# Kernel tuning notes

Measured on AMD Instinct MI355X. Metric: run time of the kernel, lower is better.

The kernel has to match this reference:

```python
import jax, jax.numpy as jnp
import numpy as np

B_, L_, DM, DI, DS, DTR, DC = 1, 2048, 2048, 4096, 16, 128, 4


def setup_inputs() -> dict:
    key = jax.random.key(0)
    ks = jax.random.split(key, 8)
    s = lambda k, shape, scale: jax.random.normal(k, shape, jnp.float32) * scale
    inp = {
        "hidden_states": s(ks[0], (B_, L_, DM), 1.0),
        "in_proj_weight": s(ks[1], (2 * DI, DM), DM ** -0.5),
        "conv1d_weight": s(ks[2], (DI, 1, DC), DC ** -0.5),
        "x_proj_weight": s(ks[3], (DTR + 2 * DS, DI), DI ** -0.5),
        "dt_proj_weight": s(ks[4], (DI, DTR), DTR ** -0.5),
        "out_proj_weight": s(ks[5], (DM, DI), DI ** -0.5),
    }
    # dt_proj_bias = inverse-softplus of dt ~ LogUniform[1e-3, 0.1] (as in init_dtprojbias)
    dt = jnp.exp(jax.random.uniform(ks[6], (DI,), jnp.float32) * (np.log(0.1) - np.log(0.001)) + np.log(0.001))
    dt = jnp.clip(dt, 1e-4, None)
    inp["dt_proj_bias"] = dt + jnp.log(-jnp.expm1(-dt))
    # A_log init: log of repeat(arange(1, d_state+1)) per d_inner row
    inp["A_log"] = jnp.log(jnp.tile(jnp.arange(1, DS + 1, dtype=jnp.float32), (DI, 1)))
    inp["D"] = jnp.ones((DI,), jnp.float32)
    return inp


def reference(hidden_states, in_proj_weight, conv1d_weight, x_proj_weight,
              dt_proj_weight, dt_proj_bias, A_log, D, out_proj_weight):
    b, l, dm = hidden_states.shape
    di, ds = A_log.shape
    # in_proj: [b,l,dm] -> xz [b, 2*di, l]
    xz = jnp.einsum('ed,bld->bel', in_proj_weight, hidden_states)
    x, z = xz[:, :di], xz[:, di:]
    # depthwise causal conv1d (pad left d_conv-1, no bias) + SiLU
    x = jax.lax.conv_general_dilated(
        x, conv1d_weight, window_strides=(1,), padding=[(DC - 1, 0)],
        dimension_numbers=('NCH', 'OIH', 'NCH'), feature_group_count=di)
    x = jax.nn.silu(x)  # [b, di, l]
    # x_proj -> dt, B, C
    x_dbl = jnp.einsum('pd,bdl->blp', x_proj_weight, x)  # [b,l,dtr+2*ds]
    dt, Bc, Cc = jnp.split(x_dbl, [DTR, DTR + ds], axis=-1)
    delta = jnp.einsum('dr,blr->bld', dt_proj_weight, dt) + dt_proj_bias
    delta = jax.nn.softplus(delta)  # delta_softplus=True, delta_bias applied
    A = -jnp.exp(A_log)  # [di, ds]
    u = jnp.transpose(x, (0, 2, 1))  # [b,l,di]

    def step(h, inputs):
        d_t, B_t, C_t, u_t = inputs  # [b,di],[b,ds],[b,ds],[b,di]
        dA = jnp.exp(d_t[..., None] * A)                      # [b,di,ds]
        h = h * dA + (d_t * u_t)[..., None] * B_t[:, None, :]  # [b,di,ds]
        y = jnp.einsum('bdn,bn->bd', h, C_t)
        return h, y

    h0 = jnp.zeros((b, di, ds), hidden_states.dtype)
    xs = (jnp.swapaxes(delta, 0, 1), jnp.swapaxes(Bc, 0, 1),
          jnp.swapaxes(Cc, 0, 1), jnp.swapaxes(u, 0, 1))
    _, ys = jax.lax.scan(step, h0, xs)          # [l,b,di]
    y = jnp.swapaxes(ys, 0, 1) + u * D          # skip term u*D
    y = y * jax.nn.silu(jnp.transpose(z, (0, 2, 1)))  # gate
    return jnp.einsum('md,bld->blm', out_proj_weight, y)
```

## Files before the change

### kernel.cpp

```cpp
#include <hip/hip_runtime.h>
#include <hip/hip_bf16.h>

#define LSEQ 2048
#define DMODEL 2048
#define DINNER 4096
#define DSTATE 16
#define DTRANK 128
#define DCONV 4
#define DXP (DTRANK + 2*DSTATE)
#define NCHUNK 64
#define LCHUNK (LSEQ / NCHUNK)
#define KSPLIT 16
#define OKS 4

using bf16 = __hip_bfloat16;
typedef __attribute__((ext_vector_type(8))) short short8;
typedef __attribute__((ext_vector_type(4))) float float4v;

__device__ __forceinline__ float b2f(bf16 v) { return __bfloat162float(v); }
__device__ __forceinline__ bf16 f2b(float v) { return __float2bfloat16(v); }
__device__ __forceinline__ float bl16(unsigned u) { return __uint_as_float(u << 16); }
__device__ __forceinline__ float bh16(unsigned u) { return __uint_as_float(u & 0xffff0000u); }

__device__ __forceinline__ short f2bs(float v) {
    bf16 b = __float2bfloat16(v);
    union { bf16 b; short s; } u; u.b = b; return u.s;
}

__device__ __forceinline__ float fsilu(float x) {
    return x * __builtin_amdgcn_rcpf(1.0f + __expf(-x));
}

__device__ __forceinline__ short8 ld8(const float* p) {
    float4v f0 = *(const float4v*)p;
    float4v f1 = *(const float4v*)(p + 4);
    short8 r;
    r[0] = f2bs(f0[0]); r[1] = f2bs(f0[1]); r[2] = f2bs(f0[2]); r[3] = f2bs(f0[3]);
    r[4] = f2bs(f1[0]); r[5] = f2bs(f1[1]); r[6] = f2bs(f1[2]); r[7] = f2bs(f1[3]);
    return r;
}
__device__ __forceinline__ short8 ld8(const bf16* p) { return *(const short8*)p; }

template<typename CT> __device__ __forceinline__ CT cvtC(float v);
template<> __device__ __forceinline__ bf16  cvtC<bf16>(float v)  { return f2b(v); }
template<> __device__ __forceinline__ float cvtC<float>(float v) { return v; }

template<typename T> __device__ __forceinline__ float cvtL(T v);
template<> __device__ __forceinline__ float cvtL<bf16>(bf16 v)   { return b2f(v); }
template<> __device__ __forceinline__ float cvtL<float>(float v) { return v; }

__device__ __forceinline__ void glds16(const bf16* g, void* lds_base) {
    __builtin_amdgcn_global_load_lds(
        (const __attribute__((address_space(1))) void*)g,
        (__attribute__((address_space(3))) void*)lds_base, 16, 0, 0);
}

__global__ __launch_bounds__(256) void cvt3(
    const float* __restrict__ s0, bf16* __restrict__ d0, int n0,
    const float* __restrict__ s1, bf16* __restrict__ d1, int n1,
    const float* __restrict__ s2, bf16* __restrict__ d2, int n2)
{
    const int b = blockIdx.x;
    const int nb0 = n0 >> 11, nb1 = n1 >> 11;
    const float* s; bf16* d; int i;
    if (b < nb0)            { s = s0; d = d0; i = b * 2048; }
    else if (b < nb0 + nb1) { s = s1; d = d1; i = (b - nb0) * 2048; }
    else                    { s = s2; d = d2; i = (b - nb0 - nb1) * 2048; }
    i += threadIdx.x * 8;
    *(short8*)(d + i) = ld8(s + i);
}

__global__ __launch_bounds__(256) void cvt1(
    const float* __restrict__ src, bf16* __restrict__ dst, int n)
{
    int i = (blockIdx.x * 256 + threadIdx.x) * 8;
    if (i >= n) return;
    *(short8*)(dst + i) = ld8(src + i);
}

#define GBAR  __builtin_amdgcn_s_barrier()
#define VMW4  asm volatile("s_waitcnt vmcnt(4)" ::: "memory")
#define VMW0  asm volatile("s_waitcnt vmcnt(0)" ::: "memory")

#define LDA8(BASE, RB, AF) do {                                                \
  _Pragma("unroll") for (int mi_ = 0; mi_ < 4; ++mi_)                          \
  _Pragma("unroll") for (int kk_ = 0; kk_ < 2; ++kk_)                          \
    AF[mi_][kk_] = *(const short8*)((BASE) + (((RB) + mi_*16 + t16) << 6)      \
                                    + ((((kk_*4) + quad) ^ sw7) << 3));        \
} while (0)

#define LDB4(BASE, RB, BF) do {                                                \
  _Pragma("unroll") for (int nj_ = 0; nj_ < 2; ++nj_)                          \
  _Pragma("unroll") for (int kk_ = 0; kk_ < 2; ++kk_)                          \
    BF[nj_][kk_] = *(const short8*)((BASE) + (((RB) + nj_*16 + t16) << 6)      \
                                    + ((((kk_*4) + quad) ^ sw7) << 3));        \
} while (0)

#define MM16(AF, BF, MO, NO) do {                                              \
  _Pragma("unroll") for (int kk_ = 0; kk_ < 2; ++kk_)                          \
  _Pragma("unroll") for (int mi_ = 0; mi_ < 4; ++mi_)                          \
  _Pragma("unroll") for (int nj_ = 0; nj_ < 2; ++nj_)                          \
    acc[(MO)+mi_][(NO)+nj_] = __builtin_amdgcn_mfma_f32_16x16x32_bf16(         \
        AF[mi_][kk_], BF[nj_][kk_], acc[(MO)+mi_][(NO)+nj_], 0, 0, 0);         \
} while (0)

#define ST_ALO(tau) do { size_t ko_ = (size_t)(tau) << 6; int bo_ = ((tau)&1) << 15; \
  glds16(sA +       ko_, dA0 + bo_);                                           \
  glds16(sA + oA1 + ko_, dA1 + bo_); } while (0)
#define ST_AHI(tau) do { size_t ko_ = (size_t)(tau) << 6; int bo_ = ((tau)&1) << 15; \
  glds16(sA + oA2 + ko_, dA2 + bo_);                                           \
  glds16(sA + oA3 + ko_, dA3 + bo_); } while (0)
#define ST_BLO(tau) do { size_t ko_ = (size_t)(tau) << 6; int bo_ = ((tau)&1) << 15; \
  glds16(sB +       ko_, dB0 + bo_);                                           \
  glds16(sB + oB1 + ko_, dB1 + bo_); } while (0)
#define ST_BHI(tau) do { size_t ko_ = (size_t)(tau) << 6; int bo_ = ((tau)&1) << 15; \
  glds16(sB + oB2 + ko_, dB2 + bo_);                                           \
  glds16(sB + oB3 + ko_, dB3 + bo_); } while (0)

#define KSTEP(T, BI) do {                                                      \
    const bf16* Ab = As[BI];                                                   \
    const bf16* Bb = Bs[BI];                                                   \
    short8 af[4][2], b0[2][2], b1[2][2];                                       \
                                       \
    LDA8(Ab, wm, af);                                                          \
    LDB4(Bb, wn, b0);                                                          \
    if ((T) + 1 < NT) { ST_AHI((T) + 1); ST_BLO((T) + 1); }                    \
    __builtin_amdgcn_s_setprio(1); MM16(af, b0, 0, 0);                         \
    __builtin_amdgcn_s_setprio(0); GBAR;                                       \
                    \
    LDB4(Bb, wn + 32, b1);                                                     \
    if ((T) + 2 < NT) ST_ALO((T) + 2);                                         \
    __builtin_amdgcn_s_setprio(1); MM16(af, b1, 0, 2);                         \
    __builtin_amdgcn_s_setprio(0); GBAR;                                       \
                           \
    LDA8(Ab, wm + 64, af);                                                     \
    if ((T) + 2 < NT) ST_BHI((T) + 2);                                         \
    __builtin_amdgcn_s_setprio(1); MM16(af, b1, 4, 2);                         \
    __builtin_amdgcn_s_setprio(0); GBAR;                                       \
                                   \
    __builtin_amdgcn_s_setprio(1); MM16(af, b0, 4, 0);                         \
    __builtin_amdgcn_s_setprio(0);                                             \
    if ((T) + 2 < NT) { VMW4; } else { VMW0; }                                 \
    GBAR;                                                                      \
} while (0)

#define GEMM_PRO_COMMON                                                        \
    const int t    = threadIdx.x;                                              \
    const int wave = t >> 6;                                                   \
    const int lane = t & 63;                                                   \
    const int t16  = lane & 15;                                                \
    const int quad = lane >> 4;                                                \
    const int sw7  = t16 & 7;                                                  \
    const int wm   = (wave >> 2) * 128;                                        \
    const int wn   = (wave & 3) * 64;                                          \
    const int lrow  = lane >> 3;                                               \
    const int lseg  = lane & 7;                                                \
    const int segx  = (lseg ^ lrow) * 8;                                       \
    const int bwoff = (wave & 3) * 8 + (wave >> 2) * 64;

#define GEMM_LDS_DSTS                                                          \
    char* dA0 = (char*)&As[0][(  0 + wave * 8) * 64];                          \
    char* dA1 = (char*)&As[0][(128 + wave * 8) * 64];                          \
    char* dA2 = (char*)&As[0][( 64 + wave * 8) * 64];                          \
    char* dA3 = (char*)&As[0][(192 + wave * 8) * 64];                          \
    char* dB0 = (char*)&Bs[0][(  0 + bwoff) * 64];                             \
    char* dB1 = (char*)&Bs[0][(128 + bwoff) * 64];                             \
    char* dB2 = (char*)&Bs[0][( 32 + bwoff) * 64];                             \
    char* dB3 = (char*)&Bs[0][(160 + bwoff) * 64];

__global__ __launch_bounds__(512, 2) void gemm_inproj(
    const bf16* __restrict__ A, int lda,
    const bf16* __restrict__ B, int ldb,
    bf16* __restrict__ C, int ldc, int K)
{
    __shared__ __align__(16) bf16 As[2][256 * 64];
    __shared__ __align__(16) bf16 Bs[2][256 * 64];
    GEMM_PRO_COMMON
    const int bid = blockIdx.x;
    const int s   = (bid & 7) * (gridDim.x >> 3) + (bid >> 3);
    const int bm0 = (s & 7) << 8;
    const int bn0 = (s >> 3) << 8;

    const bf16* sA = A + (size_t)(bm0 + wave * 8 + lrow) * lda + segx;
    const bf16* sB = B + (size_t)(bn0 + bwoff + lrow) * ldb + segx;
    const size_t oA1 = (size_t)128 * lda, oA2 = (size_t)64 * lda, oA3 = (size_t)192 * lda;
    const size_t oB1 = (size_t)128 * ldb, oB2 = (size_t)32 * ldb, oB3 = (size_t)160 * ldb;
    GEMM_LDS_DSTS

    const int NT = K >> 6;

    float4v acc[8][4];
#pragma unroll
    for (int i = 0; i < 8; ++i)
#pragma unroll
        for (int j = 0; j < 4; ++j) acc[i][j] = (float4v)(0.0f);

    ST_ALO(0); ST_AHI(0); ST_BLO(0); ST_BHI(0);
    if (NT > 1) { ST_ALO(1); ST_BHI(1); VMW4; } else { VMW0; }
    GBAR;

    for (int T = 0; T < NT; T += 2) {
        KSTEP(T, 0);
        KSTEP(T + 1, 1);
    }

#pragma unroll
    for (int mi = 0; mi < 8; ++mi) {
#pragma unroll
        for (int nj = 0; nj < 4; ++nj) {
            const int m_base = bm0 + wm + (mi >> 2) * 64 + (mi & 3) * 16 + quad * 4;
            const int n_g    = bn0 + wn + (nj >> 1) * 32 + (nj & 1) * 16 + t16;
#pragma unroll
            for (int r = 0; r < 4; ++r)
                C[(size_t)(m_base + r) * ldc + n_g] = f2b(acc[mi][nj][r]);
        }
    }
}

__global__ __launch_bounds__(512, 2) void gemm_outproj(
    const bf16* __restrict__ A, int lda,
    const bf16* __restrict__ B, int ldb,
    float* __restrict__ P, int ldc, int Kc)
{
    __shared__ __align__(16) bf16 As[2][256 * 64];
    __shared__ __align__(16) bf16 Bs[2][256 * 64];
    GEMM_PRO_COMMON
    const int bid = blockIdx.x;
    const int s   = (bid & 7) * (gridDim.x >> 3) + (bid >> 3);
    const int bm0 = (s & 7) << 8;
    const int t2  = s >> 3;
    const int bn0 = (t2 & 7) << 8;
    const int ks  = t2 >> 3;

    const bf16* sA = A + (size_t)(bm0 + wave * 8 + lrow) * lda + segx + (size_t)ks * Kc;
    const bf16* sB = B + (size_t)(bn0 + bwoff + lrow) * ldb + segx + (size_t)ks * Kc;
    const size_t oA1 = (size_t)128 * lda, oA2 = (size_t)64 * lda, oA3 = (size_t)192 * lda;
    const size_t oB1 = (size_t)128 * ldb, oB2 = (size_t)32 * ldb, oB3 = (size_t)160 * ldb;
    GEMM_LDS_DSTS

    const int NT = Kc >> 6;

    float4v acc[8][4];
#pragma unroll
    for (int i = 0; i < 8; ++i)
#pragma unroll
        for (int j = 0; j < 4; ++j) acc[i][j] = (float4v)(0.0f);

    ST_ALO(0); ST_AHI(0); ST_BLO(0); ST_BHI(0);
    if (NT > 1) { ST_ALO(1); ST_BHI(1); VMW4; } else { VMW0; }
    GBAR;

    for (int T = 0; T < NT; T += 2) {
        KSTEP(T, 0);
        KSTEP(T + 1, 1);
    }

    float* Pk = P + (size_t)ks * 2048 * (size_t)ldc;
#pragma unroll
    for (int mi = 0; mi < 8; ++mi) {
#pragma unroll
        for (int nj = 0; nj < 4; ++nj) {
            const int m_base = bm0 + wm + (mi >> 2) * 64 + (mi & 3) * 16 + quad * 4;
            const int n_g    = bn0 + wn + (nj >> 1) * 32 + (nj & 1) * 16 + t16;
#pragma unroll
            for (int r = 0; r < 4; ++r)
                Pk[(size_t)(m_base + r) * ldc + n_g] = acc[mi][nj][r];
        }
    }
}

__global__ __launch_bounds__(256) void reduce4f(
    const float* __restrict__ P, float* __restrict__ out, int MN)
{
    int i = (blockIdx.x * 256 + threadIdx.x) * 4;
    if (i >= MN) return;
    float4v s = *(const float4v*)(P + i);
#pragma unroll
    for (int ks = 1; ks < OKS; ++ks) {
        float4v v = *(const float4v*)(P + (size_t)ks * MN + i);
#pragma unroll
        for (int j = 0; j < 4; ++j) s[j] += v[j];
    }
    *(float4v*)(out + i) = s;
}

template<int BN, typename CT, bool SP>
__global__ __launch_bounds__(256) void gemm_glds64(
    const bf16* __restrict__ A, int lda,
    const bf16* __restrict__ B, int ldb,
    CT* __restrict__ C, int ldc,
    int K, const float* __restrict__ bias)
{
    constexpr int NJ  = BN / 32;
    constexpr int BGL = BN / 32;
    __shared__ bf16 As[128][64];
    __shared__ bf16 Bs[BN][64];

    const int t    = threadIdx.x;
    const int wave = t >> 6;
    const int lane = t & 63;
    const int t16  = lane & 15;
    const int quad = lane >> 4;
    const int wm   = (wave >> 1) * 64;
    const int wn   = (wave & 1) * (BN / 2);
    const int bm0  = blockIdx.x * 128;
    const int bn0  = blockIdx.y * BN;

    const int lrow = lane >> 3;
    const int gseg = (((lane & 7) ^ lrow) * 8);

    const bf16* Ag[4]; char* Ad[4];
#pragma unroll
    for (int g = 0; g < 4; g++) {
        Ag[g] = A + (size_t)(bm0 + wave * 32 + g * 8 + lrow) * lda + gseg;
        Ad[g] = (char*)As + (wave * 32 + g * 8) * 128;
    }
    const bf16* Bg[BGL]; char* Bd[BGL];
#pragma unroll
    for (int g = 0; g < BGL; g++) {
        int r = (BN == 128) ? (wave * 32 + g * 8) : (wave * 16 + g * 8);
        Bg[g] = B + (size_t)(bn0 + r + lrow) * ldb + gseg;
        Bd[g] = (char*)Bs + r * 128;
    }

    float4v acc[4][NJ];
#pragma unroll
    for (int i = 0; i < 4; i++)
#pragma unroll
        for (int j = 0; j < NJ; j++) acc[i][j] = (float4v)(0.0f);

    const int sw = t16 & 7;

    for (int k0 = 0; k0 < K; k0 += 64) {
        __syncthreads();
#pragma unroll
        for (int g = 0; g < 4; g++)   glds16(Ag[g] + k0, Ad[g]);
#pragma unroll
        for (int g = 0; g < BGL; g++) glds16(Bg[g] + k0, Bd[g]);
        __syncthreads();

#pragma unroll
        for (int kk = 0; kk < 2; kk++) {
            const int kso = ((kk * 4 + quad) ^ sw) * 8;
            short8 a[4], b[NJ];
#pragma unroll
            for (int mi = 0; mi < 4; mi++)
                a[mi] = *(const short8*)(&As[wm + mi * 16 + t16][kso]);
#pragma unroll
            for (int nj = 0; nj < NJ; nj++)
                b[nj] = *(const short8*)(&Bs[wn + nj * 16 + t16][kso]);
#pragma unroll
            for (int mi = 0; mi < 4; mi++)
#pragma unroll
                for (int nj = 0; nj < NJ; nj++)
                    acc[mi][nj] = __builtin_amdgcn_mfma_f32_16x16x32_bf16(
                        a[mi], b[nj], acc[mi][nj], 0, 0, 0);
        }
    }

#pragma unroll
    for (int mi = 0; mi < 4; mi++) {
#pragma unroll
        for (int nj = 0; nj < NJ; nj++) {
            int n_g = bn0 + wn + nj * 16 + t16;
            float bia = SP ? bias[n_g] : 0.0f;
#pragma unroll
            for (int r = 0; r < 4; r++) {
                int m_g = bm0 + wm + mi * 16 + quad * 4 + r;
                float v = acc[mi][nj][r];
                if (SP) {
                    float x = v + bia;
                    v = (x > 20.0f) ? x : __logf(1.0f + __expf(x));
                }
                C[(size_t)m_g * ldc + n_g] = cvtC<CT>(v);
            }
        }
    }
}

template<typename AT, typename CT, bool SP>
__global__ __launch_bounds__(256) void gemm_bt(
    const AT* __restrict__ A, int lda,
    const float* __restrict__ B, int ldb,
    CT* __restrict__ C, int ldc,
    int M, int N, int K,
    const float* __restrict__ bias)
{
    __shared__ bf16 As[64][40];
    __shared__ bf16 Bs[64][40];

    const int t    = threadIdx.x;
    const int bm0  = blockIdx.x * 64;
    const int bn0  = blockIdx.y * 64;
    const int row  = t >> 2;
    const int seg  = (t & 3) * 8;
    const int wave = t >> 6;
    const int lane = t & 63;
    const int wm   = (wave >> 1) * 32;
    const int wn   = (wave & 1) * 32;
    const int t16  = lane & 15;
    const int quad = lane >> 4;

    float4v acc[2][2];
#pragma unroll
    for (int i = 0; i < 2; i++)
#pragma unroll
        for (int j = 0; j < 2; j++) acc[i][j] = (float4v)(0.0f);

    const AT*    Aptr = A + (size_t)(bm0 + row) * lda + seg;
    const float* Bptr = B + (size_t)(bn0 + row) * ldb + seg;
    const bool a_ok = (bm0 + row) < M;
    const bool b_ok = (bn0 + row) < N;
    const short8 zero8 = (short8)(0);

    for (int k0 = 0; k0 < K; k0 += 32) {
        short8 av = a_ok ? ld8(Aptr + k0) : zero8;
        short8 bv = b_ok ? ld8(Bptr + k0) : zero8;
        __syncthreads();
        *(short8*)(&As[row][seg]) = av;
        *(short8*)(&Bs[row][seg]) = bv;
        __syncthreads();

        short8 a0 = *(const short8*)(&As[wm + t16][quad * 8]);
        short8 a1 = *(const short8*)(&As[wm + 16 + t16][quad * 8]);
        short8 b0 = *(const short8*)(&Bs[wn + t16][quad * 8]);
        short8 b1 = *(const short8*)(&Bs[wn + 16 + t16][quad * 8]);
        acc[0][0] = __builtin_amdgcn_mfma_f32_16x16x32_bf16(a0, b0, acc[0][0], 0, 0, 0);
        acc[0][1] = __builtin_amdgcn_mfma_f32_16x16x32_bf16(a0, b1, acc[0][1], 0, 0, 0);
        acc[1][0] = __builtin_amdgcn_mfma_f32_16x16x32_bf16(a1, b0, acc[1][0], 0, 0, 0);
        acc[1][1] = __builtin_amdgcn_mfma_f32_16x16x32_bf16(a1, b1, acc[1][1], 0, 0, 0);
    }

#pragma unroll
    for (int i = 0; i < 2; i++) {
#pragma unroll
        for (int j = 0; j < 2; j++) {
            int n_g = bn0 + wn + j * 16 + t16;
            if (n_g >= N) continue;
            float bia = SP ? bias[n_g] : 0.0f;
#pragma unroll
            for (int r = 0; r < 4; r++) {
                int m_g = bm0 + wm + i * 16 + quad * 4 + r;
                if (m_g >= M) continue;
                float v = acc[i][j][r];
                if (SP) {
                    float x = v + bia;
                    v = (x > 20.0f) ? x : log1pf(__expf(x));
                }
                C[(size_t)m_g * ldc + n_g] = cvtC<CT>(v);
            }
        }
    }
}

__global__ __launch_bounds__(256) void gemm_bt_splitk(
    const bf16* __restrict__ A, int lda,
    const float* __restrict__ B, int ldb,
    float* __restrict__ P,
    int M, int N, int K)
{
    __shared__ bf16 As[64][40];
    __shared__ bf16 Bs[64][40];

    const int t    = threadIdx.x;
    const int bm0  = blockIdx.x * 64;
    const int bn0  = blockIdx.y * 64;
    const int ks   = blockIdx.z;
    const int KS   = gridDim.z;
    const int kbeg = ks * (K / KS);
    const int kend = kbeg + (K / KS);
    const int row  = t >> 2;
    const int seg  = (t & 3) * 8;
    const int wave = t >> 6;
    const int lane = t & 63;
    const int wm   = (wave >> 1) * 32;
    const int wn   = (wave & 1) * 32;
    const int t16  = lane & 15;
    const int quad = lane >> 4;

    float4v acc[2][2];
#pragma unroll
    for (int i = 0; i < 2; i++)
#pragma unroll
        for (int j = 0; j < 2; j++) acc[i][j] = (float4v)(0.0f);

    const bf16*  Aptr = A + (size_t)(bm0 + row) * lda + seg;
    const float* Bptr = B + (size_t)(bn0 + row) * ldb + seg;
    const bool a_ok = (bm0 + row) < M;
    const bool b_ok = (bn0 + row) < N;
    const short8 zero8 = (short8)(0);

    for (int k0 = kbeg; k0 < kend; k0 += 32) {
        short8 av = a_ok ? ld8(Aptr + k0) : zero8;
        short8 bv = b_ok ? ld8(Bptr + k0) : zero8;
        __syncthreads();
        *(short8*)(&As[row][seg]) = av;
        *(short8*)(&Bs[row][seg]) = bv;
        __syncthreads();

        short8 a0 = *(const short8*)(&As[wm + t16][quad * 8]);
        short8 a1 = *(const short8*)(&As[wm + 16 + t16][quad * 8]);
        short8 b0 = *(const short8*)(&Bs[wn + t16][quad * 8]);
        short8 b1 = *(const short8*)(&Bs[wn + 16 + t16][quad * 8]);
        acc[0][0] = __builtin_amdgcn_mfma_f32_16x16x32_bf16(a0, b0, acc[0][0], 0, 0, 0);
        acc[0][1] = __builtin_amdgcn_mfma_f32_16x16x32_bf16(a0, b1, acc[0][1], 0, 0, 0);
        acc[1][0] = __builtin_amdgcn_mfma_f32_16x16x32_bf16(a1, b0, acc[1][0], 0, 0, 0);
        acc[1][1] = __builtin_amdgcn_mfma_f32_16x16x32_bf16(a1, b1, acc[1][1], 0, 0, 0);
    }

    float* Pk = P + (size_t)ks * M * N;
#pragma unroll
    for (int i = 0; i < 2; i++) {
#pragma unroll
        for (int j = 0; j < 2; j++) {
            int n_g = bn0 + wn + j * 16 + t16;
            if (n_g >= N) continue;
#pragma unroll
            for (int r = 0; r < 4; r++) {
                int m_g = bm0 + wm + i * 16 + quad * 4 + r;
                if (m_g >= M) continue;
                Pk[(size_t)m_g * N + n_g] = acc[i][j][r];
            }
        }
    }
}

__global__ __launch_bounds__(256) void reduce_splitk(
    const float* __restrict__ P, bf16* __restrict__ C, float* __restrict__ bc, int MN)
{
    int i = blockIdx.x * 256 + threadIdx.x;
    if (i >= MN) return;
    float s = 0.f;
#pragma unroll
    for (int ks = 0; ks < KSPLIT; ks++) s += P[(size_t)ks * MN + i];
    C[i] = f2b(s);
    int l = i / DXP;
    int p = i - l * DXP;
    if (p >= DTRANK) bc[l * 32 + (p - DTRANK)] = s;
}

__global__ __launch_bounds__(256) void conv_silu_par(
    const bf16* __restrict__ xz, const float* __restrict__ w, bf16* __restrict__ xc)
{
    const int d  = blockIdx.x * 256 + threadIdx.x;
    const int lc = blockIdx.y * 256;
    const float w0 = w[d * 4 + 0];
    const float w1 = w[d * 4 + 1];
    const float w2 = w[d * 4 + 2];
    const float w3 = w[d * 4 + 3];
    const size_t S = 2 * DINNER;
    const bf16* p = xz + d;
    float xm3 = 0.f, xm2 = 0.f, xm1 = 0.f;
    if (lc >= 3) {
        xm3 = b2f(p[(size_t)(lc - 3) * S]);
        xm2 = b2f(p[(size_t)(lc - 2) * S]);
        xm1 = b2f(p[(size_t)(lc - 1) * S]);
    }
    for (int l = lc; l < lc + 256; ++l) {
        float x0 = b2f(p[(size_t)l * S]);
        float a = w0 * xm3 + w1 * xm2 + w2 * xm1 + w3 * x0;
        xc[(size_t)l * DINNER + d] = f2b(fsilu(a));
        xm3 = xm2; xm2 = xm1; xm1 = x0;
    }
}

__global__ __launch_bounds__(256) void conv_silu_inplace(
    bf16* __restrict__ xz, const float* __restrict__ w)
{
    const int d = blockIdx.x * 256 + threadIdx.x;
    const float w0 = w[d * 4 + 0];
    const float w1 = w[d * 4 + 1];
    const float w2 = w[d * 4 + 2];
    const float w3 = w[d * 4 + 3];
    bf16* p = xz + d;
    const size_t S = 2 * DINNER;
    float xm3 = 0.f, xm2 = 0.f, xm1 = 0.f;
    for (int l = 0; l < LSEQ; l += 4) {
        float x0 = b2f(p[(size_t)(l + 0) * S]);
        float x1 = b2f(p[(size_t)(l + 1) * S]);
        float x2 = b2f(p[(size_t)(l + 2) * S]);
        float x3 = b2f(p[(size_t)(l + 3) * S]);
        float a0 = w0 * xm3 + w1 * xm2 + w2 * xm1 + w3 * x0;
        float a1 = w0 * xm2 + w1 * xm1 + w2 * x0  + w3 * x1;
        float a2 = w0 * xm1 + w1 * x0  + w2 * x1  + w3 * x2;
        float a3 = w0 * x0  + w1 * x1  + w2 * x2  + w3 * x3;
        p[(size_t)(l + 0) * S] = f2b(a0 / (1.0f + __expf(-a0)));
        p[(size_t)(l + 1) * S] = f2b(a1 / (1.0f + __expf(-a1)));
        p[(size_t)(l + 2) * S] = f2b(a2 / (1.0f + __expf(-a2)));
        p[(size_t)(l + 3) * S] = f2b(a3 / (1.0f + __expf(-a3)));
        xm3 = x1; xm2 = x2; xm1 = x3;
    }
}

__global__ __launch_bounds__(256) void scan_chunk1(
    const float* __restrict__ dlt, const bf16* __restrict__ xc,
    const float* __restrict__ bc, const float* __restrict__ A_log,
    float* __restrict__ hend, float* __restrict__ Pbuf)
{
    const int d = blockIdx.x * 256 + threadIdx.x;
    const int c = blockIdx.y;

    float Ac[16];
    {
        const float* ap = A_log + d * DSTATE;
#pragma unroll
        for (int i = 0; i < 16; i++) Ac[i] = -__expf(ap[i]);
    }

    float h[16];
#pragma unroll
    for (int i = 0; i < 16; i++) h[i] = 0.f;
    float sdelta = 0.f;

    const float* pd = dlt + (size_t)c * LCHUNK * DINNER + d;
    const bf16*  pu = xc  + (size_t)c * LCHUNK * DINNER + d;
    const float* pb = bc  + (size_t)c * LCHUNK * 32;

#pragma unroll 2
    for (int l = 0; l < LCHUNK; ++l) {
        const float delta = *pd;
        const float u     = b2f(*pu);
        const float du    = delta * u;
        sdelta += delta;
        float4v B0 = *(const float4v*)pb;
        float4v B1 = *(const float4v*)(pb + 4);
        float4v B2 = *(const float4v*)(pb + 8);
        float4v B3 = *(const float4v*)(pb + 12);
#pragma unroll
        for (int i = 0; i < 16; i++) {
            float dA = __expf(delta * Ac[i]);
            float Bi = (i < 4) ? B0[i] : (i < 8) ? B1[i - 4] : (i < 12) ? B2[i - 8] : B3[i - 12];
            h[i] = h[i] * dA + du * Bi;
        }
        pd += DINNER; pu += DINNER; pb += 32;
    }

    float* hp = hend + ((size_t)c * DINNER + d) * DSTATE;
    float* pp = Pbuf + ((size_t)c * DINNER + d) * DSTATE;
#pragma unroll
    for (int q = 0; q < 4; q++) {
        float4v hv, pv;
#pragma unroll
        for (int j = 0; j < 4; j++) {
            hv[j] = h[q * 4 + j];
            pv[j] = __expf(sdelta * Ac[q * 4 + j]);
        }
        *(float4v*)(hp + q * 4) = hv;
        *(float4v*)(pp + q * 4) = pv;
    }
}

__global__ __launch_bounds__(256) void scan_combine(
    float* __restrict__ hend, const float* __restrict__ Pbuf)
{
    const int dn = blockIdx.x * 256 + threadIdx.x;
    const size_t STR = (size_t)DINNER * DSTATE;
    float H = 0.f;
    size_t idx = dn;
    for (int c0 = 0; c0 < NCHUNK; c0 += 8) {
        float he[8], pp[8];
#pragma unroll
        for (int j = 0; j < 8; j++) {
            he[j] = hend[idx + (size_t)j * STR];
            pp[j] = Pbuf[idx + (size_t)j * STR];
        }
#pragma unroll
        for (int j = 0; j < 8; j++) {
            hend[idx + (size_t)j * STR] = H;
            H = he[j] + pp[j] * H;
        }
        idx += 8 * STR;
    }
}

__global__ __launch_bounds__(256) void scan_chunk2(
    const float* __restrict__ dlt, const bf16* __restrict__ xc,
    bf16* __restrict__ xz, const float* __restrict__ bc,
    const float* __restrict__ A_log, const float* __restrict__ Dp,
    const float* __restrict__ Hin)
{
    const int d = blockIdx.x * 256 + threadIdx.x;
    const int c = blockIdx.y;

    float Ac[16];
    {
        const float* ap = A_log + d * DSTATE;
#pragma unroll
        for (int i = 0; i < 16; i++) Ac[i] = -__expf(ap[i]);
    }
    const float Dv = Dp[d];

    float h[16];
    {
        const float* hp = Hin + ((size_t)c * DINNER + d) * DSTATE;
#pragma unroll
        for (int q = 0; q < 4; q++) {
            float4v hv = *(const float4v*)(hp + q * 4);
#pragma unroll
            for (int j = 0; j < 4; j++) h[q * 4 + j] = hv[j];
        }
    }

    const float* pd = dlt + (size_t)c * LCHUNK * DINNER + d;
    const bf16*  pu = xc  + (size_t)c * LCHUNK * DINNER + d;
    const float* pb = bc  + (size_t)c * LCHUNK * 32;
    bf16*        pz = xz  + (size_t)c * LCHUNK * (2 * DINNER) + DINNER + d;

#pragma unroll 2
    for (int l = 0; l < LCHUNK; ++l) {
        const float delta = *pd;
        const float u     = b2f(*pu);
        const float du    = delta * u;
        float4v B0 = *(const float4v*)pb;
        float4v B1 = *(const float4v*)(pb + 4);
        float4v B2 = *(const float4v*)(pb + 8);
        float4v B3 = *(const float4v*)(pb + 12);
        float4v C0 = *(const float4v*)(pb + 16);
        float4v C1 = *(const float4v*)(pb + 20);
        float4v C2 = *(const float4v*)(pb + 24);
        float4v C3 = *(const float4v*)(pb + 28);
        float yv = 0.f;
#pragma unroll
        for (int i = 0; i < 16; i++) {
            float dA = __expf(delta * Ac[i]);
            float Bi = (i < 4) ? B0[i] : (i < 8) ? B1[i - 4] : (i < 12) ? B2[i - 8] : B3[i - 12];
            float Ci = (i < 4) ? C0[i] : (i < 8) ? C1[i - 4] : (i < 12) ? C2[i - 8] : C3[i - 12];
            h[i] = h[i] * dA + du * Bi;
            yv += h[i] * Ci;
        }
        yv += u * Dv;
        float z = b2f(*pz);
        yv *= fsilu(z);
        *pz = f2b(yv);
        pd += DINNER; pu += DINNER; pb += 32; pz += 2 * DINNER;
    }
}

template<typename DT>
__global__ __launch_bounds__(256) void scan_serial(
    const DT* __restrict__ dlt, bf16* __restrict__ xz,
    const bf16* __restrict__ xdbl,
    const float* __restrict__ A_log, const float* __restrict__ Dp)
{
    const int nq = threadIdx.x & 3;
    const int d  = blockIdx.x * 64 + (threadIdx.x >> 2);
    float Ac[4];
#pragma unroll
    for (int i = 0; i < 4; i++)
        Ac[i] = -__expf(A_log[d * DSTATE + nq * 4 + i]);
    const float Dv = Dp[d];
    float h[4] = {0.f, 0.f, 0.f, 0.f};
    for (int l = 0; l < LSEQ; ++l) {
        const float delta = cvtL<DT>(dlt[(size_t)l * DINNER + d]);
        const float u     = b2f(xz[(size_t)l * (2 * DINNER) + d]);
        const uint2 qb = *(const uint2*)(xdbl + (size_t)l * DXP + DTRANK + nq * 4);
        const uint2 qc = *(const uint2*)(xdbl + (size_t)l * DXP + DTRANK + DSTATE + nq * 4);
        float Bv[4] = { bl16(qb.x), bh16(qb.x), bl16(qb.y), bh16(qb.y) };
        float Cv[4] = { bl16(qc.x), bh16(qc.x), bl16(qc.y), bh16(qc.y) };
        const float du = delta * u;
        float yv = 0.f;
#pragma unroll
        for (int i = 0; i < 4; i++) {
            float dA = __expf(delta * Ac[i]);
            h[i] = h[i] * dA + du * Bv[i];
            yv += h[i] * Cv[i];
        }
        yv += __shfl_xor(yv, 1);
        yv += __shfl_xor(yv, 2);
        if (nq == 0) {
            yv += u * Dv;
            bf16* zp = xz + (size_t)l * (2 * DINNER) + DINNER + d;
            float z = b2f(*zp);
            yv *= z / (1.0f + __expf(-z));
            *zp = f2b(yv);
        }
    }
}

extern "C" void kernel_launch(void* const* d_in, const int* in_sizes, int n_in,
                              void* d_out, int out_size, void* d_ws, size_t ws_size,
                              hipStream_t stream)
{
    const float* hs      = (const float*)d_in[0];
    const float* w_in    = (const float*)d_in[1];
    const float* w_conv  = (const float*)d_in[2];
    const float* w_xproj = (const float*)d_in[3];
    const float* w_dt    = (const float*)d_in[4];
    const float *w_out, *b_dt, *A_log, *Dp;
    if (in_sizes[5] == DMODEL * DINNER) {
        w_out = (const float*)d_in[5];
        b_dt  = (const float*)d_in[6];
        A_log = (const float*)d_in[7];
        Dp    = (const float*)d_in[8];
    } else {
        b_dt  = (const float*)d_in[5];
        A_log = (const float*)d_in[6];
        Dp    = (const float*)d_in[7];
        w_out = (const float*)d_in[8];
    }
    float* out = (float*)d_out;

    const size_t SZ_XZ   = (size_t)LSEQ * 2 * DINNER * sizeof(bf16);
    const size_t SZ_XC   = (size_t)LSEQ * DINNER * sizeof(bf16);
    const size_t SZ_XDBL = (size_t)LSEQ * DXP * sizeof(bf16);
    const size_t SZ_DLTF = (size_t)LSEQ * DINNER * sizeof(float);
    const size_t SZ_HP   = (size_t)NCHUNK * DINNER * DSTATE * sizeof(float);
    const size_t SZ_BC   = (size_t)LSEQ * 32 * sizeof(float);

    char* p = (char*)d_ws;
    bf16* xz = (bf16*)p; p += SZ_XZ;

    const size_t need_fast = SZ_XZ + SZ_XC + SZ_XDBL + SZ_DLTF + 2 * SZ_HP + SZ_BC;
    const bool fast = ws_size >= need_fast;

    dim3 blk(256);

    if (fast) {
        bf16*  xc   = (bf16*)p;  p += SZ_XC;
        bf16*  xdbl = (bf16*)p;  p += SZ_XDBL;
        char*  hpr  = p;         p += SZ_DLTF;
        char*  dreg = p;
        float* dlt  = (float*)hpr;
        float* hend = (float*)dreg;
        float* Pbuf = (float*)(dreg + SZ_HP);
        float* bcb  = (float*)(dreg + 2 * SZ_HP);

        bf16*  w_in_b  = (bf16*)hpr;
        float* xp_part = (float*)hpr;
        bf16*  hs_b    = (bf16*)dreg;
        bf16*  w_dt_b  = (bf16*)(dreg + (size_t)LSEQ * DMODEL * sizeof(bf16));
        bf16*  w_out_b = (bf16*)xc;
        float* p_out   = (float*)hpr;

        {
            int n0 = 2 * DINNER * DMODEL, n1 = LSEQ * DMODEL, n2 = DINNER * DTRANK;
            cvt3<<<dim3((n0 + n1 + n2) / 2048), blk, 0, stream>>>(
                w_in, w_in_b, n0, hs, hs_b, n1, w_dt, w_dt_b, n2);
        }

        gemm_inproj<<<dim3(256), dim3(512), 0, stream>>>(
            hs_b, DMODEL, w_in_b, DMODEL, xz, 2*DINNER, DMODEL);

        conv_silu_par<<<dim3(DINNER/256, LSEQ/256), blk, 0, stream>>>(xz, w_conv, xc);

        gemm_bt_splitk<<<dim3(LSEQ/64, 3, KSPLIT), blk, 0, stream>>>(
            xc, DINNER, w_xproj, DINNER, xp_part, LSEQ, DXP, DINNER);
        reduce_splitk<<<dim3((LSEQ * DXP + 255) / 256), blk, 0, stream>>>(
            xp_part, xdbl, bcb, LSEQ * DXP);

        gemm_glds64<128, float, true><<<dim3(LSEQ/128, DINNER/128), blk, 0, stream>>>(
            xdbl, DXP, w_dt_b, DTRANK, dlt, DINNER, DTRANK, b_dt);

        scan_chunk1<<<dim3(DINNER/256, NCHUNK), blk, 0, stream>>>(
            dlt, xc, bcb, A_log, hend, Pbuf);
        scan_combine<<<dim3(DINNER*DSTATE/256), blk, 0, stream>>>(hend, Pbuf);
        scan_chunk2<<<dim3(DINNER/256, NCHUNK), blk, 0, stream>>>(
            dlt, xc, xz, bcb, A_log, Dp, hend);

        cvt1<<<dim3((DMODEL*DINNER)/2048), blk, 0, stream>>>(w_out, w_out_b, DMODEL*DINNER);
        gemm_outproj<<<dim3(256), dim3(512), 0, stream>>>(
            xz + DINNER, 2*DINNER, w_out_b, DINNER, p_out, DMODEL, DINNER/OKS);
        reduce4f<<<dim3(LSEQ*DMODEL/1024), blk, 0, stream>>>(
            p_out, out, LSEQ*DMODEL);
    } else {
        bf16* xdbl = (bf16*)p; p += SZ_XDBL;
        size_t used = (size_t)(p - (char*)d_ws);
        bool dlt_f32 = (ws_size - used) >= SZ_DLTF;

        gemm_bt<float, bf16, false><<<dim3(LSEQ/64, (2*DINNER)/64), blk, 0, stream>>>(
            hs, DMODEL, w_in, DMODEL, xz, 2*DINNER, LSEQ, 2*DINNER, DMODEL, nullptr);
        conv_silu_inplace<<<dim3(DINNER/256), blk, 0, stream>>>(xz, w_conv);
        gemm_bt<bf16, bf16, false><<<dim3(LSEQ/64, 3), blk, 0, stream>>>(
            xz, 2*DINNER, w_xproj, DINNER, xdbl, DXP, LSEQ, DXP, DINNER, nullptr);
        if (dlt_f32) {
            float* dlt = (float*)p;
            gemm_bt<bf16, float, true><<<dim3(LSEQ/64, DINNER/64), blk, 0, stream>>>(
                xdbl, DXP, w_dt, DTRANK, dlt, DINNER, LSEQ, DINNER, DTRANK, b_dt);
            scan_serial<float><<<dim3(DINNER/64), blk, 0, stream>>>(dlt, xz, xdbl, A_log, Dp);
        } else {
            bf16* dlt = (bf16*)p;
            gemm_bt<bf16, bf16, true><<<dim3(LSEQ/64, DINNER/64), blk, 0, stream>>>(
                xdbl, DXP, w_dt, DTRANK, dlt, DINNER, LSEQ, DINNER, DTRANK, b_dt);
            scan_serial<bf16><<<dim3(DINNER/64), blk, 0, stream>>>(dlt, xz, xdbl, A_log, Dp);
        }
        gemm_bt<bf16, float, false><<<dim3(LSEQ/64, DMODEL/64), blk, 0, stream>>>(
            xz + DINNER, 2*DINNER, w_out, DINNER, out, DMODEL, LSEQ, DMODEL, DINNER, nullptr);
    }
}
```

Baseline: 425.8 us.

## Replace x_proj split-K GEMM with swizzled 128x160 LDS-direct kernel and bf16 weight

Replaces the small 64x64 split-K x_proj GEMM with a new kernel that tiles 128 rows by the full 160 output columns, loads A and B straight into LDS with global_load_lds and XOR swizzling, and uses a 4x5 MFMA accumulator tile per wave. This removes the wasted padded third N-tile and the per-lane fp32-to-bf16 loads. The x_proj weight is now converted to bf16 once inside the fused conversion kernel, which grows to four sources. The conv+SiLU kernel gets a finer sequence split (64 instead of 256 rows per block) for more parallelism, at the cost of extra halo reads.

```diff
diff --git a/kernel.cpp b/kernel.cpp
--- a/kernel.cpp
+++ b/kernel.cpp
@@ -55,17 +55,19 @@
         (__attribute__((address_space(3))) void*)lds_base, 16, 0, 0);
 }
 
-__global__ __launch_bounds__(256) void cvt3(
+__global__ __launch_bounds__(256) void cvt4(
     const float* __restrict__ s0, bf16* __restrict__ d0, int n0,
     const float* __restrict__ s1, bf16* __restrict__ d1, int n1,
-    const float* __restrict__ s2, bf16* __restrict__ d2, int n2)
+    const float* __restrict__ s2, bf16* __restrict__ d2, int n2,
+    const float* __restrict__ s3, bf16* __restrict__ d3, int n3)
 {
     const int b = blockIdx.x;
-    const int nb0 = n0 >> 11, nb1 = n1 >> 11;
+    const int nb0 = n0 >> 11, nb1 = n1 >> 11, nb2 = n2 >> 11;
     const float* s; bf16* d; int i;
-    if (b < nb0)            { s = s0; d = d0; i = b * 2048; }
-    else if (b < nb0 + nb1) { s = s1; d = d1; i = (b - nb0) * 2048; }
-    else                    { s = s2; d = d2; i = (b - nb0 - nb1) * 2048; }
+    if (b < nb0)                  { s = s0; d = d0; i = b * 2048; }
+    else if (b < nb0 + nb1)       { s = s1; d = d1; i = (b - nb0) * 2048; }
+    else if (b < nb0 + nb1 + nb2) { s = s2; d = d2; i = (b - nb0 - nb1) * 2048; }
+    else                          { s = s3; d = d3; i = (b - nb0 - nb1 - nb2) * 2048; }
     i += threadIdx.x * 8;
     *(short8*)(d + i) = ld8(s + i);
 }
@@ -284,6 +286,92 @@
     *(float4v*)(out + i) = s;
 }
 
+__global__ __launch_bounds__(256) void gemm_xproj(
+    const bf16* __restrict__ A, int lda,
+    const bf16* __restrict__ B, int ldb,
+    float* __restrict__ P)
+{
+    __shared__ bf16 As[128][64];
+    __shared__ bf16 Bs[160][64];
+
+    const int t    = threadIdx.x;
+    const int wave = t >> 6;
+    const int lane = t & 63;
+    const int t16  = lane & 15;
+    const int quad = lane >> 4;
+    const int wm   = (wave >> 1) * 64;
+    const int wn   = (wave & 1) * 80;
+    const int bm0  = blockIdx.x * 128;
+    const int kbeg = blockIdx.y * (DINNER / KSPLIT);
+
+    const int lrow = lane >> 3;
+    const int gseg = ((lane & 7) ^ lrow) * 8;
+
+    const bf16* Ag[4]; char* Ad[4];
+#pragma unroll
+    for (int g = 0; g < 4; g++) {
+        int r = wave * 32 + g * 8;
+        Ag[g] = A + (size_t)(bm0 + r + lrow) * lda + gseg + kbeg;
+        Ad[g] = (char*)As + r * 128;
+    }
+    const bf16* Bg[5]; char* Bd[5];
+#pragma unroll
+    for (int g = 0; g < 5; g++) {
+        int r = wave * 40 + g * 8;
+        Bg[g] = B + (size_t)(r + lrow) * ldb + gseg + kbeg;
+        Bd[g] = (char*)Bs + r * 128;
+    }
+
+    float4v acc[4][5];
+#pragma unroll
+    for (int i = 0; i < 4; i++)
+#pragma unroll
+        for (int j = 0; j < 5; j++) acc[i][j] = (float4v)(0.0f);
+
+    const int sw = t16 & 7;
+
+    for (int k0 = 0; k0 < DINNER / KSPLIT; k0 += 64) {
+        __syncthreads();
+#pragma unroll
+        for (int g = 0; g < 4; g++) glds16(Ag[g] + k0, Ad[g]);
+#pragma unroll
+        for (int g = 0; g < 5; g++) glds16(Bg[g] + k0, Bd[g]);
+        __syncthreads();
+
+#pragma unroll
+        for (int kk = 0; kk < 2; kk++) {
+            const int kso = ((kk * 4 + quad) ^ sw) * 8;
+            short8 a[4], b[5];
+#pragma unroll
+            for (int mi = 0; mi < 4; mi++)
+                a[mi] = *(const short8*)(&As[wm + mi * 16 + t16][kso]);
+#pragma unroll
+            for (int nj = 0; nj < 5; nj++)
+                b[nj] = *(const short8*)(&Bs[wn + nj * 16 + t16][kso]);
+#pragma unroll
+            for (int mi = 0; mi < 4; mi++)
+#pragma unroll
+                for (int nj = 0; nj < 5; nj++)
+                    acc[mi][nj] = __builtin_amdgcn_mfma_f32_16x16x32_bf16(
+                        a[mi], b[nj], acc[mi][nj], 0, 0, 0);
+        }
+    }
+
+    float* Pk = P + (size_t)blockIdx.y * LSEQ * DXP;
+#pragma unroll
+    for (int mi = 0; mi < 4; mi++) {
+#pragma unroll
+        for (int nj = 0; nj < 5; nj++) {
+            int n_g = wn + nj * 16 + t16;
+#pragma unroll
+            for (int r = 0; r < 4; r++) {
+                int m_g = bm0 + wm + mi * 16 + quad * 4 + r;
+                Pk[(size_t)m_g * DXP + n_g] = acc[mi][nj][r];
+            }
+        }
+    }
+}
+
 template<int BN, typename CT, bool SP>
 __global__ __launch_bounds__(256) void gemm_glds64(
     const bf16* __restrict__ A, int lda,
@@ -453,78 +541,6 @@
     }
 }
 
-__global__ __launch_bounds__(256) void gemm_bt_splitk(
-    const bf16* __restrict__ A, int lda,
-    const float* __restrict__ B, int ldb,
-    float* __restrict__ P,
-    int M, int N, int K)
-{
-    __shared__ bf16 As[64][40];
-    __shared__ bf16 Bs[64][40];
-
-    const int t    = threadIdx.x;
-    const int bm0  = blockIdx.x * 64;
-    const int bn0  = blockIdx.y * 64;
-    const int ks   = blockIdx.z;
-    const int KS   = gridDim.z;
-    const int kbeg = ks * (K / KS);
-    const int kend = kbeg + (K / KS);
-    const int row  = t >> 2;
-    const int seg  = (t & 3) * 8;
-    const int wave = t >> 6;
-    const int lane = t & 63;
-    const int wm   = (wave >> 1) * 32;
-    const int wn   = (wave & 1) * 32;
-    const int t16  = lane & 15;
-    const int quad = lane >> 4;
-
-    float4v acc[2][2];
-#pragma unroll
-    for (int i = 0; i < 2; i++)
-#pragma unroll
-        for (int j = 0; j < 2; j++) acc[i][j] = (float4v)(0.0f);
-
-    const bf16*  Aptr = A + (size_t)(bm0 + row) * lda + seg;
-    const float* Bptr = B + (size_t)(bn0 + row) * ldb + seg;
-    const bool a_ok = (bm0 + row) < M;
-    const bool b_ok = (bn0 + row) < N;
-    const short8 zero8 = (short8)(0);
-
-    for (int k0 = kbeg; k0 < kend; k0 += 32) {
-        short8 av = a_ok ? ld8(Aptr + k0) : zero8;
-        short8 bv = b_ok ? ld8(Bptr + k0) : zero8;
-        __syncthreads();
-        *(short8*)(&As[row][seg]) = av;
-        *(short8*)(&Bs[row][seg]) = bv;
-        __syncthreads();
-
-        short8 a0 = *(const short8*)(&As[wm + t16][quad * 8]);
-        short8 a1 = *(const short8*)(&As[wm + 16 + t16][quad * 8]);
-        short8 b0 = *(const short8*)(&Bs[wn + t16][quad * 8]);
-        short8 b1 = *(const short8*)(&Bs[wn + 16 + t16][quad * 8]);
-        acc[0][0] = __builtin_amdgcn_mfma_f32_16x16x32_bf16(a0, b0, acc[0][0], 0, 0, 0);
-        acc[0][1] = __builtin_amdgcn_mfma_f32_16x16x32_bf16(a0, b1, acc[0][1], 0, 0, 0);
-        acc[1][0] = __builtin_amdgcn_mfma_f32_16x16x32_bf16(a1, b0, acc[1][0], 0, 0, 0);
-        acc[1][1] = __builtin_amdgcn_mfma_f32_16x16x32_bf16(a1, b1, acc[1][1], 0, 0, 0);
-    }
-
-    float* Pk = P + (size_t)ks * M * N;
-#pragma unroll
-    for (int i = 0; i < 2; i++) {
-#pragma unroll
-        for (int j = 0; j < 2; j++) {
-            int n_g = bn0 + wn + j * 16 + t16;
-            if (n_g >= N) continue;
-#pragma unroll
-            for (int r = 0; r < 4; r++) {
-                int m_g = bm0 + wm + i * 16 + quad * 4 + r;
-                if (m_g >= M) continue;
-                Pk[(size_t)m_g * N + n_g] = acc[i][j][r];
-            }
-        }
-    }
-}
-
 __global__ __launch_bounds__(256) void reduce_splitk(
     const float* __restrict__ P, bf16* __restrict__ C, float* __restrict__ bc, int MN)
 {
@@ -543,7 +559,7 @@
     const bf16* __restrict__ xz, const float* __restrict__ w, bf16* __restrict__ xc)
 {
     const int d  = blockIdx.x * 256 + threadIdx.x;
-    const int lc = blockIdx.y * 256;
+    const int lc = blockIdx.y * 64;
     const float w0 = w[d * 4 + 0];
     const float w1 = w[d * 4 + 1];
     const float w2 = w[d * 4 + 2];
@@ -556,7 +572,7 @@
         xm2 = b2f(p[(size_t)(lc - 2) * S]);
         xm1 = b2f(p[(size_t)(lc - 1) * S]);
     }
-    for (int l = lc; l < lc + 256; ++l) {
+    for (int l = lc; l < lc + 64; ++l) {
         float x0 = b2f(p[(size_t)l * S]);
         float a = w0 * xm3 + w1 * xm2 + w2 * xm1 + w3 * x0;
         xc[(size_t)l * DINNER + d] = f2b(fsilu(a));
@@ -829,22 +845,25 @@
         float* xp_part = (float*)hpr;
         bf16*  hs_b    = (bf16*)dreg;
         bf16*  w_dt_b  = (bf16*)(dreg + (size_t)LSEQ * DMODEL * sizeof(bf16));
+        bf16*  w_xp_b  = (bf16*)(dreg + (size_t)LSEQ * DMODEL * sizeof(bf16)
+                                      + (size_t)DINNER * DTRANK * sizeof(bf16));
         bf16*  w_out_b = (bf16*)xc;
         float* p_out   = (float*)hpr;
 
         {
-            int n0 = 2 * DINNER * DMODEL, n1 = LSEQ * DMODEL, n2 = DINNER * DTRANK;
-            cvt3<<<dim3((n0 + n1 + n2) / 2048), blk, 0, stream>>>(
-                w_in, w_in_b, n0, hs, hs_b, n1, w_dt, w_dt_b, n2);
+            int n0 = 2 * DINNER * DMODEL, n1 = LSEQ * DMODEL;
+            int n2 = DINNER * DTRANK,     n3 = DXP * DINNER;
+            cvt4<<<dim3((n0 + n1 + n2 + n3) / 2048), blk, 0, stream>>>(
+                w_in, w_in_b, n0, hs, hs_b, n1, w_dt, w_dt_b, n2, w_xproj, w_xp_b, n3);
         }
 
         gemm_inproj<<<dim3(256), dim3(512), 0, stream>>>(
             hs_b, DMODEL, w_in_b, DMODEL, xz, 2*DINNER, DMODEL);
 
-        conv_silu_par<<<dim3(DINNER/256, LSEQ/256), blk, 0, stream>>>(xz, w_conv, xc);
-
-        gemm_bt_splitk<<<dim3(LSEQ/64, 3, KSPLIT), blk, 0, stream>>>(
-            xc, DINNER, w_xproj, DINNER, xp_part, LSEQ, DXP, DINNER);
+        conv_silu_par<<<dim3(DINNER/256, LSEQ/64), blk, 0, stream>>>(xz, w_conv, xc);
+
+        gemm_xproj<<<dim3(LSEQ/128, KSPLIT), blk, 0, stream>>>(
+            xc, DINNER, w_xp_b, DINNER, xp_part);
         reduce_splitk<<<dim3((LSEQ * DXP + 255) / 256), blk, 0, stream>>>(
             xp_part, xdbl, bcb, LSEQ * DXP);
 
```

Result: faster. 401.2 us (-5.8%).
